# Kernel tuning notes

Hardware: AMD Instinct MI355X
Metric: run time of the kernel (lower is better)

The kernel has to match this reference:

```python
import jax, jax.numpy as jnp
import numpy as np

N_NODES = 50000
N_EDGES = 400000
D = 128
N_BASIS = 8


def setup_inputs() -> dict:
    key = jax.random.key(0)
    ks = jax.random.split(key, 12)
    p1 = jax.random.normal(ks[0], (N_NODES, D), dtype=jnp.float32)
    idx_i = jax.random.randint(ks[1], (N_EDGES,), 0, N_NODES, dtype=jnp.int32)
    idx_j = jax.random.randint(ks[2], (N_EDGES,), 0, N_NODES, dtype=jnp.int32)
    basis = jax.random.normal(ks[3], (N_EDGES, N_BASIS), dtype=jnp.float32)
    s = 0.05
    # pp MLP: [128,128,128] -> two Linear layers with tanh
    pp_w1 = jax.random.normal(ks[4], (D, D), dtype=jnp.float32) * s
    pp_b1 = jnp.zeros((D,), dtype=jnp.float32)
    pp_w2 = jax.random.normal(ks[5], (D, D), dtype=jnp.float32) * s
    pp_b2 = jnp.zeros((D,), dtype=jnp.float32)
    # pi Linear: 2D -> D*n_basis (no activation)
    pi_w = jax.random.normal(ks[6], (2 * D, D * N_BASIS), dtype=jnp.float32) * s
    pi_b = jnp.zeros((D * N_BASIS,), dtype=jnp.float32)
    # ii MLP: [128,128] -> one Linear with tanh
    ii_w = jax.random.normal(ks[7], (D, D), dtype=jnp.float32) * s
    ii_b = jnp.zeros((D,), dtype=jnp.float32)
    return {
        "p1": p1, "idx_i": idx_i, "idx_j": idx_j, "basis": basis,
        "pp_w1": pp_w1, "pp_b1": pp_b1, "pp_w2": pp_w2, "pp_b2": pp_b2,
        "pi_w": pi_w, "pi_b": pi_b, "ii_w": ii_w, "ii_b": ii_b,
    }


def reference(p1, idx_i, idx_j, basis,
              pp_w1, pp_b1, pp_w2, pp_b2,
              pi_w, pi_b, ii_w, ii_b):
    # pp_layer: node MLP with tanh activations
    h = jnp.tanh(p1 @ pp_w1 + pp_b1)          # [N, D]
    h = jnp.tanh(h @ pp_w2 + pp_b2)           # [N, D]
    # pi_layer: gather endpoints, concat, linear (no activation)
    inter = jnp.concatenate([h[idx_i], h[idx_j]], axis=-1)  # [E, 2D]
    inter = inter @ pi_w + pi_b                              # [E, D*B]
    inter = inter.reshape(-1, D, N_BASIS)                    # [E, D, B]
    inter = jnp.einsum("pcb,pb->pc", inter, basis)          # [E, D]
    # ii_layer: edge MLP with tanh
    i1 = jnp.tanh(inter @ ii_w + ii_b)                       # [E, D]
    # ip_layer: scatter_add over idx_j back to nodes
    out = jax.ops.segment_sum(i1, idx_j, num_segments=p1.shape[0])  # [N, D]
    return out
```

## Files before the change

kernel.cpp:

```cpp
#include <hip/hip_runtime.h>

typedef __attribute__((ext_vector_type(8))) short short8;
typedef __attribute__((ext_vector_type(4))) float f32x4;

__device__ inline ushort f2bf(float f) {
  union { float f; unsigned u; } v; v.f = f;
  return (ushort)((v.u + 0x7fffu + ((v.u >> 16) & 1u)) >> 16);
}

__device__ inline float fast_tanh(float x) {
  float ax = __builtin_fabsf(x);
  float u = __builtin_amdgcn_exp2f(-2.8853900817779268f * ax);
  float r = (1.0f - u) * __builtin_amdgcn_rcpf(1.0f + u);
  return __builtin_copysignf(r, x);
}

__global__ __launch_bounds__(256)
void prep_weights(const float* __restrict__ pi_w, const float* __restrict__ ii_w,
                  ushort* __restrict__ Wtp, ushort* __restrict__ iiWtp)
{
  int tid = blockIdx.x * 256 + threadIdx.x;
  if (tid < 64 * 8 * 64 * 8) {
    int m = tid & 7, lane = (tid >> 3) & 63, ks = (tid >> 9) & 7, nt = tid >> 12;
    int k = ks * 32 + (lane >> 4) * 8 + m;
    int n = nt * 16 + (lane & 15);
    Wtp[tid] = f2bf(pi_w[k * 1024 + n]);
  } else {
    int t = tid - 262144;
    if (t < 8 * 4 * 64 * 8) {
      int m = t & 7, lane = (t >> 3) & 63, ks = (t >> 9) & 3, dt = t >> 11;
      int c = ks * 32 + (lane >> 4) * 8 + m;
      int d = dt * 16 + (lane & 15);
      iiWtp[t] = f2bf(ii_w[c * 128 + d]);
    }
  }
}

__global__ __launch_bounds__(256)
void pp_kernel(const float* __restrict__ p1,
               const float* __restrict__ w1, const float* __restrict__ b1,
               const float* __restrict__ w2, const float* __restrict__ b2,
               ushort* __restrict__ hbf, int N)
{
  __shared__ float p1s[32 * 128];
  __shared__ float h1s[32 * 128];
  const int tid = threadIdx.x;
  const int n0 = blockIdx.x * 32;

  #pragma unroll
  for (int p = 0; p < 4; ++p) {
    int off = (p * 256 + tid) * 4;
    int n = n0 + (off >> 7);
    float4 v = make_float4(0.f, 0.f, 0.f, 0.f);
    if (n < N) v = *(const float4*)(p1 + (size_t)n0 * 128 + off);
    *(float4*)(p1s + off) = v;
  }
  __syncthreads();

  const int c = tid & 127;
  const int nset = tid >> 7;
  float acc[16];

  #pragma unroll
  for (int n = 0; n < 16; ++n) acc[n] = b1[c];
  for (int k = 0; k < 128; k += 4) {
    float wa = w1[(k + 0) * 128 + c];
    float wb = w1[(k + 1) * 128 + c];
    float wc = w1[(k + 2) * 128 + c];
    float wd = w1[(k + 3) * 128 + c];
    #pragma unroll
    for (int n = 0; n < 16; ++n) {
      const float4 pv = *(const float4*)(p1s + (nset * 16 + n) * 128 + k);
      acc[n] += pv.x * wa + pv.y * wb + pv.z * wc + pv.w * wd;
    }
  }
  #pragma unroll
  for (int n = 0; n < 16; ++n) h1s[(nset * 16 + n) * 128 + c] = fast_tanh(acc[n]);
  __syncthreads();

  #pragma unroll
  for (int n = 0; n < 16; ++n) acc[n] = b2[c];
  for (int k = 0; k < 128; k += 4) {
    float wa = w2[(k + 0) * 128 + c];
    float wb = w2[(k + 1) * 128 + c];
    float wc = w2[(k + 2) * 128 + c];
    float wd = w2[(k + 3) * 128 + c];
    #pragma unroll
    for (int n = 0; n < 16; ++n) {
      const float4 pv = *(const float4*)(h1s + (nset * 16 + n) * 128 + k);
      acc[n] += pv.x * wa + pv.y * wb + pv.z * wc + pv.w * wd;
    }
  }
  #pragma unroll
  for (int n = 0; n < 16; ++n) {
    int node = n0 + nset * 16 + n;
    if (node < N) hbf[(size_t)node * 128 + c] = f2bf(fast_tanh(acc[n]));
  }
}

__global__ __launch_bounds__(256, 3)
void edge_kernel(const ushort* __restrict__ hbf,
                 const int* __restrict__ idx_i, const int* __restrict__ idx_j,
                 const float* __restrict__ basis,
                 const ushort* __restrict__ Wtp,
                 const float* __restrict__ pi_b,
                 const ushort* __restrict__ iiWtp,
                 const float* __restrict__ ii_b,
                 float* __restrict__ out, int E)
{
  __shared__ ushort Xs[48 * 256];
  __shared__ ushort Ys[48 * 128];
  __shared__ alignas(16) float basis_s[48 * 8];
  __shared__ int idxj_s[48];

  const int tid = threadIdx.x;
  const int wave = tid >> 6;
  const int lane = tid & 63;
  const int lane16 = lane & 15;
  const int lgrp = lane >> 4;
  const size_t e0 = (size_t)blockIdx.x * 48;
  const size_t elim = (size_t)E - 1;

  #pragma unroll
  for (int pass = 0; pass < 6; ++pass) {
    int r = pass * 16 + (tid >> 4);
    int l16 = tid & 15;
    int e = r >> 1;
    size_t eg = e0 + e; if (eg > elim) eg = elim;
    int node = (r & 1) ? idx_j[eg] : idx_i[eg];
    int4 v = *(const int4*)(hbf + (size_t)node * 128 + l16 * 8);
    int kb = ((r & 1) * 128 + l16 * 8) * 2;
    *(int4*)((char*)Xs + e * 512 + (kb ^ ((e & 7) << 4))) = v;
  }
  {
    size_t blim = (size_t)E * 8 - 1;
    size_t i1 = e0 * 8 + tid;        if (i1 > blim) i1 = blim;
    basis_s[tid] = basis[i1];
    if (tid < 128) {
      size_t i2 = e0 * 8 + 256 + tid; if (i2 > blim) i2 = blim;
      basis_s[256 + tid] = basis[i2];
    }
    if (tid < 48) {
      size_t eg = e0 + tid; if (eg > elim) eg = elim;
      idxj_s[tid] = idx_j[eg];
    }
  }
  __syncthreads();

  short8 xf[3][8];
  #pragma unroll
  for (int et = 0; et < 3; ++et) {
    int e = et * 16 + lane16;
    #pragma unroll
    for (int ks = 0; ks < 8; ++ks) {
      xf[et][ks] = *(const short8*)((const char*)Xs + e * 512 + ((ks * 64 + lgrp * 16) ^ ((e & 7) << 4)));
      asm volatile("" : "+v"(xf[et][ks]));
    }
  }
  float4 bas[3];
  #pragma unroll
  for (int et = 0; et < 3; ++et) {
    int e = et * 16 + lane16;
    bas[et] = *(const float4*)((const char*)basis_s + e * 32 + (lgrp & 1) * 16);
  }

  #pragma unroll
  for (int ct = 0; ct < 16; ++ct) {
    const int ntg = wave * 16 + ct;
    const float4 pib = *(const float4*)(pi_b + ntg * 16 + lgrp * 4);
    f32x4 acc[3];
    #pragma unroll
    for (int et = 0; et < 3; ++et)
      acc[et] = (f32x4){pib.x, pib.y, pib.z, pib.w};
    #pragma unroll
    for (int ks = 0; ks < 8; ++ks) {
      short8 a = *(const short8*)(Wtp + ((size_t)(ntg * 8 + ks) * 64 + lane) * 8);
      #pragma unroll
      for (int et = 0; et < 3; ++et)
        acc[et] = __builtin_amdgcn_mfma_f32_16x16x32_bf16(a, xf[et][ks], acc[et], 0, 0, 0);
    }
    const int cg = ntg * 2 + (lgrp >> 1);
    #pragma unroll
    for (int et = 0; et < 3; ++et) {
      int e = et * 16 + lane16;
      float part = acc[et][0] * bas[et].x + acc[et][1] * bas[et].y
                 + acc[et][2] * bas[et].z + acc[et][3] * bas[et].w;
      part += __shfl_xor(part, 16);
      if (!(lgrp & 1))
        *(ushort*)((char*)Ys + e * 256 + ((cg * 2) ^ ((e & 7) << 4))) = f2bf(part);
    }
  }
  __syncthreads();

  short8 yf[3][4];
  #pragma unroll
  for (int et = 0; et < 3; ++et) {
    int e = et * 16 + lane16;
    #pragma unroll
    for (int ks = 0; ks < 4; ++ks)
      yf[et][ks] = *(const short8*)((const char*)Ys + e * 256 + ((ks * 64 + lgrp * 16) ^ ((e & 7) << 4)));
  }

  f32x4 acc2[3][2];
  #pragma unroll
  for (int et = 0; et < 3; ++et)
    #pragma unroll
    for (int dtl = 0; dtl < 2; ++dtl)
      acc2[et][dtl] = (f32x4){0.f, 0.f, 0.f, 0.f};

  #pragma unroll
  for (int dtl = 0; dtl < 2; ++dtl) {
    const int dtg = wave * 2 + dtl;
    #pragma unroll
    for (int ks = 0; ks < 4; ++ks) {
      short8 a = *(const short8*)(iiWtp + ((size_t)(dtg * 4 + ks) * 64 + lane) * 8);
      #pragma unroll
      for (int et = 0; et < 3; ++et)
        acc2[et][dtl] = __builtin_amdgcn_mfma_f32_16x16x32_bf16(a, yf[et][ks], acc2[et][dtl], 0, 0, 0);
    }
  }

  float4 iib[2];
  #pragma unroll
  for (int dtl = 0; dtl < 2; ++dtl)
    iib[dtl] = *(const float4*)(ii_b + (wave * 2 + dtl) * 16 + lgrp * 4);

  float* Tr = (float*)Xs;
  #pragma unroll
  for (int dtl = 0; dtl < 2; ++dtl) {
    int d0 = (wave * 2 + dtl) * 16 + lgrp * 4;
    #pragma unroll
    for (int et = 0; et < 3; ++et) {
      int e = et * 16 + lane16;
      float4 v;
      v.x = fast_tanh(acc2[et][dtl][0] + iib[dtl].x);
      v.y = fast_tanh(acc2[et][dtl][1] + iib[dtl].y);
      v.z = fast_tanh(acc2[et][dtl][2] + iib[dtl].z);
      v.w = fast_tanh(acc2[et][dtl][3] + iib[dtl].w);
      *(float4*)((char*)Tr + e * 512 + ((d0 * 4) ^ ((e & 7) << 4))) = v;
    }
  }
  __syncthreads();

  {
    const int c = tid & 127;
    const int eb = tid >> 7;
    #pragma unroll
    for (int p = 0; p < 24; ++p) {
      int e = eb + p * 2;
      if (e0 + e < (size_t)E) {
        float v = *(const float*)((const char*)Tr + e * 512 + ((c * 4) ^ ((e & 7) << 4)));
        unsafeAtomicAdd(out + (size_t)idxj_s[e] * 128 + c, v);
      }
    }
  }
}

extern "C" void kernel_launch(void* const* d_in, const int* in_sizes, int n_in,
                              void* d_out, int out_size, void* d_ws, size_t ws_size,
                              hipStream_t stream)
{
  const float* p1    = (const float*)d_in[0];
  const int*   idx_i = (const int*)d_in[1];
  const int*   idx_j = (const int*)d_in[2];
  const float* basis = (const float*)d_in[3];
  const float* pp_w1 = (const float*)d_in[4];
  const float* pp_b1 = (const float*)d_in[5];
  const float* pp_w2 = (const float*)d_in[6];
  const float* pp_b2 = (const float*)d_in[7];
  const float* pi_w  = (const float*)d_in[8];
  const float* pi_b  = (const float*)d_in[9];
  const float* ii_w  = (const float*)d_in[10];
  const float* ii_b  = (const float*)d_in[11];

  const int N = in_sizes[0] / 128;
  const int E = in_sizes[1];

  ushort* hbf   = (ushort*)d_ws;
  ushort* Wtp   = (ushort*)((char*)d_ws + (size_t)N * 128 * 2);
  ushort* iiWtp = (ushort*)((char*)Wtp + (size_t)262144 * 2);

  hipMemsetAsync(d_out, 0, (size_t)out_size * sizeof(float), stream);

  prep_weights<<<dim3((262144 + 16384) / 256), dim3(256), 0, stream>>>(
      pi_w, ii_w, Wtp, iiWtp);
  pp_kernel<<<dim3((N + 31) / 32), dim3(256), 0, stream>>>(
      p1, pp_w1, pp_b1, pp_w2, pp_b2, hbf, N);
  edge_kernel<<<dim3((E + 47) / 48), dim3(256), 0, stream>>>(
      hbf, idx_i, idx_j, basis, Wtp, pi_b, iiWtp, ii_b, (float*)d_out, E);
}
```

Measured before the change: 404.4 us.

## Port node MLP to bf16 MFMA and specialize full/tail blocks

Rewrites the node MLP kernel to use bf16 MFMA with pre-packed weights instead of scalar FP32 FMAs, staging 64 nodes per block in swizzled LDS. Splits both the node and edge kernels into a bounds-free full-block launch and a single tail-block launch. Adds s_setprio around MFMA loops. Inputs to the first layer are rounded to bf16, slightly lowering precision.

```diff
diff --git a/kernel.cpp b/kernel.cpp
--- a/kernel.cpp
+++ b/kernel.cpp
@@ -17,87 +17,120 @@
 
 __global__ __launch_bounds__(256)
 void prep_weights(const float* __restrict__ pi_w, const float* __restrict__ ii_w,
-                  ushort* __restrict__ Wtp, ushort* __restrict__ iiWtp)
+                  const float* __restrict__ pp_w1, const float* __restrict__ pp_w2,
+                  ushort* __restrict__ Wtp, ushort* __restrict__ iiWtp,
+                  ushort* __restrict__ ppW1p, ushort* __restrict__ ppW2p)
 {
   int tid = blockIdx.x * 256 + threadIdx.x;
-  if (tid < 64 * 8 * 64 * 8) {
+  if (tid < 262144) {
     int m = tid & 7, lane = (tid >> 3) & 63, ks = (tid >> 9) & 7, nt = tid >> 12;
     int k = ks * 32 + (lane >> 4) * 8 + m;
     int n = nt * 16 + (lane & 15);
     Wtp[tid] = f2bf(pi_w[k * 1024 + n]);
   } else {
     int t = tid - 262144;
-    if (t < 8 * 4 * 64 * 8) {
-      int m = t & 7, lane = (t >> 3) & 63, ks = (t >> 9) & 3, dt = t >> 11;
-      int c = ks * 32 + (lane >> 4) * 8 + m;
-      int d = dt * 16 + (lane & 15);
-      iiWtp[t] = f2bf(ii_w[c * 128 + d]);
-    }
-  }
-}
-
+    int m = t & 7, lane = (t >> 3) & 63, ks = (t >> 9) & 3, ct = (t >> 11) & 7;
+    int k = ks * 32 + (lane >> 4) * 8 + m;
+    int c = ct * 16 + (lane & 15);
+    int which = t >> 14;
+    if (which == 0)      iiWtp[t]           = f2bf(ii_w[k * 128 + c]);
+    else if (which == 1) ppW1p[t - 16384]   = f2bf(pp_w1[k * 128 + c]);
+    else                 ppW2p[t - 32768]   = f2bf(pp_w2[k * 128 + c]);
+  }
+}
+
+template <bool FULL>
 __global__ __launch_bounds__(256)
-void pp_kernel(const float* __restrict__ p1,
-               const float* __restrict__ w1, const float* __restrict__ b1,
-               const float* __restrict__ w2, const float* __restrict__ b2,
-               ushort* __restrict__ hbf, int N)
+void pp_mfma_kernel(const float* __restrict__ p1,
+                    const ushort* __restrict__ W1p, const float* __restrict__ b1,
+                    const ushort* __restrict__ W2p, const float* __restrict__ b2,
+                    ushort* __restrict__ hbf, int N, int blk0)
 {
-  __shared__ float p1s[32 * 128];
-  __shared__ float h1s[32 * 128];
+  __shared__ ushort Xs2[64 * 128];
   const int tid = threadIdx.x;
-  const int n0 = blockIdx.x * 32;
+  const int wave = tid >> 6;
+  const int lane = tid & 63;
+  const int lane16 = lane & 15;
+  const int lgrp = lane >> 4;
+  const int n0 = (blk0 + (int)blockIdx.x) * 64;
+
+  #pragma unroll
+  for (int p = 0; p < 8; ++p) {
+    int fi = p * 256 + tid;
+    int n = fi >> 5;
+    int k0 = (fi & 31) * 4;
+    int gn = n0 + n;
+    if (!FULL) gn = gn < N ? gn : N - 1;
+    float4 v = *(const float4*)(p1 + (size_t)gn * 128 + k0);
+    ushort4 u;
+    u.x = f2bf(v.x); u.y = f2bf(v.y); u.z = f2bf(v.z); u.w = f2bf(v.w);
+    *(ushort4*)((char*)Xs2 + n * 256 + ((k0 * 2) ^ ((n & 7) << 4))) = u;
+  }
+  __syncthreads();
+
+  const ushort* Wp = W1p;
+  const float* bp = b1;
+  #pragma unroll
+  for (int layer = 0; layer < 2; ++layer) {
+    short8 xf2[4][4];
+    #pragma unroll
+    for (int et = 0; et < 4; ++et) {
+      int n = et * 16 + lane16;
+      #pragma unroll
+      for (int ks = 0; ks < 4; ++ks)
+        xf2[et][ks] = *(const short8*)((const char*)Xs2 + n * 256 + ((ks * 64 + lgrp * 16) ^ ((n & 7) << 4)));
+    }
+    ushort4 uo[2][4];
+    #pragma unroll
+    for (int ct = 0; ct < 2; ++ct) {
+      const int ctg = wave * 2 + ct;
+      const float4 bb = *(const float4*)(bp + ctg * 16 + lgrp * 4);
+      f32x4 acc[4];
+      #pragma unroll
+      for (int et = 0; et < 4; ++et) acc[et] = (f32x4){bb.x, bb.y, bb.z, bb.w};
+      __builtin_amdgcn_s_setprio(1);
+      #pragma unroll
+      for (int ks = 0; ks < 4; ++ks) {
+        short8 a = *(const short8*)(Wp + ((size_t)(ctg * 4 + ks) * 64 + lane) * 8);
+        #pragma unroll
+        for (int et = 0; et < 4; ++et)
+          acc[et] = __builtin_amdgcn_mfma_f32_16x16x32_bf16(a, xf2[et][ks], acc[et], 0, 0, 0);
+      }
+      __builtin_amdgcn_s_setprio(0);
+      #pragma unroll
+      for (int et = 0; et < 4; ++et) {
+        uo[ct][et].x = f2bf(fast_tanh(acc[et][0]));
+        uo[ct][et].y = f2bf(fast_tanh(acc[et][1]));
+        uo[ct][et].z = f2bf(fast_tanh(acc[et][2]));
+        uo[ct][et].w = f2bf(fast_tanh(acc[et][3]));
+      }
+    }
+    __syncthreads();
+    #pragma unroll
+    for (int ct = 0; ct < 2; ++ct) {
+      int c0 = (wave * 2 + ct) * 16 + lgrp * 4;
+      #pragma unroll
+      for (int et = 0; et < 4; ++et) {
+        int n = et * 16 + lane16;
+        *(ushort4*)((char*)Xs2 + n * 256 + ((c0 * 2) ^ ((n & 7) << 4))) = uo[ct][et];
+      }
+    }
+    __syncthreads();
+    Wp = W2p; bp = b2;
+  }
 
   #pragma unroll
   for (int p = 0; p < 4; ++p) {
-    int off = (p * 256 + tid) * 4;
-    int n = n0 + (off >> 7);
-    float4 v = make_float4(0.f, 0.f, 0.f, 0.f);
-    if (n < N) v = *(const float4*)(p1 + (size_t)n0 * 128 + off);
-    *(float4*)(p1s + off) = v;
-  }
-  __syncthreads();
-
-  const int c = tid & 127;
-  const int nset = tid >> 7;
-  float acc[16];
-
-  #pragma unroll
-  for (int n = 0; n < 16; ++n) acc[n] = b1[c];
-  for (int k = 0; k < 128; k += 4) {
-    float wa = w1[(k + 0) * 128 + c];
-    float wb = w1[(k + 1) * 128 + c];
-    float wc = w1[(k + 2) * 128 + c];
-    float wd = w1[(k + 3) * 128 + c];
-    #pragma unroll
-    for (int n = 0; n < 16; ++n) {
-      const float4 pv = *(const float4*)(p1s + (nset * 16 + n) * 128 + k);
-      acc[n] += pv.x * wa + pv.y * wb + pv.z * wc + pv.w * wd;
-    }
-  }
-  #pragma unroll
-  for (int n = 0; n < 16; ++n) h1s[(nset * 16 + n) * 128 + c] = fast_tanh(acc[n]);
-  __syncthreads();
-
-  #pragma unroll
-  for (int n = 0; n < 16; ++n) acc[n] = b2[c];
-  for (int k = 0; k < 128; k += 4) {
-    float wa = w2[(k + 0) * 128 + c];
-    float wb = w2[(k + 1) * 128 + c];
-    float wc = w2[(k + 2) * 128 + c];
-    float wd = w2[(k + 3) * 128 + c];
-    #pragma unroll
-    for (int n = 0; n < 16; ++n) {
-      const float4 pv = *(const float4*)(h1s + (nset * 16 + n) * 128 + k);
-      acc[n] += pv.x * wa + pv.y * wb + pv.z * wc + pv.w * wd;
-    }
-  }
-  #pragma unroll
-  for (int n = 0; n < 16; ++n) {
-    int node = n0 + nset * 16 + n;
-    if (node < N) hbf[(size_t)node * 128 + c] = f2bf(fast_tanh(acc[n]));
-  }
-}
-
+    int si = p * 256 + tid;
+    int n = si >> 4;
+    int c0 = (si & 15) * 8;
+    int4 v = *(const int4*)((const char*)Xs2 + n * 256 + ((c0 * 2) ^ ((n & 7) << 4)));
+    if (FULL || n0 + n < N)
+      *(int4*)(hbf + (size_t)(n0 + n) * 128 + c0) = v;
+  }
+}
+
+template <bool FULL>
 __global__ __launch_bounds__(256, 3)
 void edge_kernel(const ushort* __restrict__ hbf,
                  const int* __restrict__ idx_i, const int* __restrict__ idx_j,
@@ -106,7 +139,7 @@
                  const float* __restrict__ pi_b,
                  const ushort* __restrict__ iiWtp,
                  const float* __restrict__ ii_b,
-                 float* __restrict__ out, int E)
+                 float* __restrict__ out, int E, int blk0)
 {
   __shared__ ushort Xs[48 * 256];
   __shared__ ushort Ys[48 * 128];
@@ -118,7 +151,7 @@
   const int lane = tid & 63;
   const int lane16 = lane & 15;
   const int lgrp = lane >> 4;
-  const size_t e0 = (size_t)blockIdx.x * 48;
+  const size_t e0 = (size_t)(blk0 + (int)blockIdx.x) * 48;
   const size_t elim = (size_t)E - 1;
 
   #pragma unroll
@@ -126,13 +159,18 @@
     int r = pass * 16 + (tid >> 4);
     int l16 = tid & 15;
     int e = r >> 1;
-    size_t eg = e0 + e; if (eg > elim) eg = elim;
+    size_t eg = e0 + e;
+    if (!FULL) { if (eg > elim) eg = elim; }
     int node = (r & 1) ? idx_j[eg] : idx_i[eg];
     int4 v = *(const int4*)(hbf + (size_t)node * 128 + l16 * 8);
     int kb = ((r & 1) * 128 + l16 * 8) * 2;
     *(int4*)((char*)Xs + e * 512 + (kb ^ ((e & 7) << 4))) = v;
   }
-  {
+  if (FULL) {
+    basis_s[tid] = basis[e0 * 8 + tid];
+    if (tid < 128) basis_s[256 + tid] = basis[e0 * 8 + 256 + tid];
+    if (tid < 48) idxj_s[tid] = idx_j[e0 + tid];
+  } else {
     size_t blim = (size_t)E * 8 - 1;
     size_t i1 = e0 * 8 + tid;        if (i1 > blim) i1 = blim;
     basis_s[tid] = basis[i1];
@@ -172,6 +210,7 @@
     #pragma unroll
     for (int et = 0; et < 3; ++et)
       acc[et] = (f32x4){pib.x, pib.y, pib.z, pib.w};
+    __builtin_amdgcn_s_setprio(1);
     #pragma unroll
     for (int ks = 0; ks < 8; ++ks) {
       short8 a = *(const short8*)(Wtp + ((size_t)(ntg * 8 + ks) * 64 + lane) * 8);
@@ -179,6 +218,7 @@
       for (int et = 0; et < 3; ++et)
         acc[et] = __builtin_amdgcn_mfma_f32_16x16x32_bf16(a, xf[et][ks], acc[et], 0, 0, 0);
     }
+    __builtin_amdgcn_s_setprio(0);
     const int cg = ntg * 2 + (lgrp >> 1);
     #pragma unroll
     for (int et = 0; et < 3; ++et) {
@@ -208,6 +248,7 @@
     for (int dtl = 0; dtl < 2; ++dtl)
       acc2[et][dtl] = (f32x4){0.f, 0.f, 0.f, 0.f};
 
+  __builtin_amdgcn_s_setprio(1);
   #pragma unroll
   for (int dtl = 0; dtl < 2; ++dtl) {
     const int dtg = wave * 2 + dtl;
@@ -219,6 +260,7 @@
         acc2[et][dtl] = __builtin_amdgcn_mfma_f32_16x16x32_bf16(a, yf[et][ks], acc2[et][dtl], 0, 0, 0);
     }
   }
+  __builtin_amdgcn_s_setprio(0);
 
   float4 iib[2];
   #pragma unroll
@@ -248,7 +290,7 @@
     #pragma unroll
     for (int p = 0; p < 24; ++p) {
       int e = eb + p * 2;
-      if (e0 + e < (size_t)E) {
+      if (FULL || e0 + e < (size_t)E) {
         float v = *(const float*)((const char*)Tr + e * 512 + ((c * 4) ^ ((e & 7) << 4)));
         unsafeAtomicAdd(out + (size_t)idxj_s[e] * 128 + c, v);
       }
@@ -276,16 +318,29 @@
   const int N = in_sizes[0] / 128;
   const int E = in_sizes[1];
 
-  ushort* hbf   = (ushort*)d_ws;
-  ushort* Wtp   = (ushort*)((char*)d_ws + (size_t)N * 128 * 2);
-  ushort* iiWtp = (ushort*)((char*)Wtp + (size_t)262144 * 2);
+  char* wp = (char*)d_ws;
+  ushort* hbf   = (ushort*)wp;  wp += (size_t)N * 128 * 2;
+  ushort* Wtp   = (ushort*)wp;  wp += (size_t)262144 * 2;
+  ushort* iiWtp = (ushort*)wp;  wp += (size_t)16384 * 2;
+  ushort* ppW1p = (ushort*)wp;  wp += (size_t)16384 * 2;
+  ushort* ppW2p = (ushort*)wp;  wp += (size_t)16384 * 2;
 
   hipMemsetAsync(d_out, 0, (size_t)out_size * sizeof(float), stream);
 
-  prep_weights<<<dim3((262144 + 16384) / 256), dim3(256), 0, stream>>>(
-      pi_w, ii_w, Wtp, iiWtp);
-  pp_kernel<<<dim3((N + 31) / 32), dim3(256), 0, stream>>>(
-      p1, pp_w1, pp_b1, pp_w2, pp_b2, hbf, N);
-  edge_kernel<<<dim3((E + 47) / 48), dim3(256), 0, stream>>>(
-      hbf, idx_i, idx_j, basis, Wtp, pi_b, iiWtp, ii_b, (float*)d_out, E);
-}
+  prep_weights<<<dim3((262144 + 3 * 16384) / 256), dim3(256), 0, stream>>>(
+      pi_w, ii_w, pp_w1, pp_w2, Wtp, iiWtp, ppW1p, ppW2p);
+
+  const int ppFull = N / 64;
+  pp_mfma_kernel<true><<<dim3(ppFull), dim3(256), 0, stream>>>(
+      p1, ppW1p, pp_b1, ppW2p, pp_b2, hbf, N, 0);
+  if (N % 64)
+    pp_mfma_kernel<false><<<dim3(1), dim3(256), 0, stream>>>(
+        p1, ppW1p, pp_b1, ppW2p, pp_b2, hbf, N, ppFull);
+
+  const int edFull = E / 48;
+  edge_kernel<true><<<dim3(edFull), dim3(256), 0, stream>>>(
+      hbf, idx_i, idx_j, basis, Wtp, pi_b, iiWtp, ii_b, (float*)d_out, E, 0);
+  if (E % 48)
+    edge_kernel<false><<<dim3(1), dim3(256), 0, stream>>>(
+        hbf, idx_i, idx_j, basis, Wtp, pi_b, iiWtp, ii_b, (float*)d_out, E, edFull);
+}
```

Measured after the change: 354.0 us. 12.5% less time.
